# Kernel tuning notes

Hardware: AMD Instinct MI355X
Metric: run time of the kernel (lower is better)

## Reference

```python
import jax, jax.numpy as jnp
import numpy as np
import math

N_HEAD = 16
HEAD_DIM = 64
N_EMBD = 1024
EPS_RMS = 1e-5
U_L2_EPS = 1e-6

def _get_alibi_slopes(n_heads):
    def pow2(n):
        start = 2 ** (-2 ** (-(math.log2(n) - 3)))
        return [start * start ** i for i in range(n)]
    if math.log2(n_heads).is_integer():
        return pow2(n_heads)
    c = 2 ** math.floor(math.log2(n_heads))
    s = pow2(c)
    extra = _get_alibi_slopes(2 * c)
    return s + extra[0::2][: n_heads - c]

def setup_inputs() -> dict:
    key = jax.random.key(0)
    ks = jax.random.split(key, 9)
    B, T = 2, 2048
    H, D, C = N_HEAD, HEAD_DIM, N_EMBD
    x = jax.random.normal(ks[0], (B, T, C), dtype=jnp.float32)
    # Linear weights stored as [in, out] so y = x @ W
    sc = 1.0 / math.sqrt(C)
    Wq = jax.random.normal(ks[1], (C, H * D), dtype=jnp.float32) * sc
    Wk = jax.random.normal(ks[2], (C, H * D), dtype=jnp.float32) * sc
    Wv = jax.random.normal(ks[3], (C, H * D), dtype=jnp.float32) * sc
    Wproj = jax.random.normal(ks[4], (H * D, C), dtype=jnp.float32) * (0.5 / math.sqrt(C) / math.sqrt(12))
    q_rms_w = jnp.ones((D,), dtype=jnp.float32)
    k_rms_w = jnp.ones((D,), dtype=jnp.float32)
    # keygated bias params: omega init = softplus_inverse(1.0), u ~ N(0, 1/sqrt(D))
    omega = jnp.full((H,), math.log(math.expm1(1.0)), dtype=jnp.float32)
    u = jax.random.normal(ks[5], (H, D), dtype=jnp.float32) * (1.0 / math.sqrt(D))
    return {"x": x, "Wq": Wq, "Wk": Wk, "Wv": Wv, "Wproj": Wproj,
            "q_rms_w": q_rms_w, "k_rms_w": k_rms_w, "omega": omega, "u": u}

def _rmsnorm(x, w):
    var = jnp.mean(jnp.square(x), axis=-1, keepdims=True)
    return x * jax.lax.rsqrt(var + EPS_RMS) * w

def reference(x, Wq, Wk, Wv, Wproj, q_rms_w, k_rms_w, omega, u):
    B, T, C = x.shape
    H, D = N_HEAD, HEAD_DIM
    q = (x @ Wq).reshape(B, T, H, D)
    k = (x @ Wk).reshape(B, T, H, D)
    v = (x @ Wv).reshape(B, T, H, D)
    q = _rmsnorm(q, q_rms_w)
    k = _rmsnorm(k, k_rms_w)
    # key-gated additive bias
    slopes = jnp.asarray(_get_alibi_slopes(H), dtype=jnp.float32)  # [H]
    omega_eff = jax.nn.softplus(omega) * slopes                    # [H]
    u_n = u / jnp.maximum(jnp.linalg.norm(u, axis=-1, keepdims=True), U_L2_EPS)
    gate_logits = jnp.einsum('bthd,hd->bht', k, u_n) / math.sqrt(D)  # fp32
    gate = jax.nn.softplus(gate_logits)                            # [B,H,T]
    idx = jnp.arange(T)
    dist = jnp.maximum(idx[:, None] - idx[None, :], 0).astype(jnp.float32)  # [T,T]
    bias = -dist[None, None] * omega_eff[None, :, None, None] * gate[:, :, None, :]  # [B,H,T,T]
    causal = idx[:, None] >= idx[None, :]
    bias = jnp.where(causal[None, None], bias, -jnp.inf)
    # attention
    scale = 1.0 / math.sqrt(D)
    scores = jnp.einsum('bihd,bjhd->bhij', q, k) * scale + bias
    attn = jax.nn.softmax(scores, axis=-1)
    y = jnp.einsum('bhij,bjhd->bihd', attn, v).reshape(B, T, H * D)
    return y @ Wproj
```

## Files before the change

kernel.cpp:

```cpp
#include <hip/hip_runtime.h>
#include <hip/hip_bf16.h>

#define NH 16
#define HD 64
#define CE 1024
#define TT 2048
#define BB 2
#define MR (BB*TT)
#define SWZ(r) ((((r) & 7)) ^ (((r) >> 3) & 3))
#define LOG2E 1.44269504f

typedef __attribute__((ext_vector_type(4))) float f32x4;
typedef __attribute__((ext_vector_type(16))) float f32x16;
typedef __attribute__((ext_vector_type(8))) short s16x8;
typedef unsigned int u32;
typedef unsigned short u16;

__device__ __forceinline__ void gld16(const void* g, void* l) {
  __builtin_amdgcn_global_load_lds((const __attribute__((address_space(1))) unsigned int*)g,
                                   (__attribute__((address_space(3))) unsigned int*)l, 16, 0, 0);
}
__device__ __forceinline__ u16 f2b(float f) {
  union { __hip_bfloat16 b; u16 u; } t;
  t.b = __float2bfloat16(f);
  return t.u;
}
__device__ __forceinline__ u32 pk2(float a, float b) {
  return (u32)f2b(a) | ((u32)f2b(b) << 16);
}
__device__ __forceinline__ float red64_sum(float v) {
#pragma unroll
  for (int m = 1; m < 64; m <<= 1) v += __shfl_xor(v, m, 64);
  return v;
}
__device__ __forceinline__ float softplusf(float x) {
  return x > 20.0f ? x : log1pf(expf(x));
}

__global__ __launch_bounds__(256) void cvt_x(const float* __restrict__ x,
                                             u16* __restrict__ xb, int n4) {
  int stride = gridDim.x * blockDim.x;
  for (int i = blockIdx.x * blockDim.x + threadIdx.x; i < n4; i += stride) {
    float4 v = ((const float4*)x)[i];
    union { u16 u[4]; uint2 p; } o;
    o.u[0] = f2b(v.x); o.u[1] = f2b(v.y); o.u[2] = f2b(v.z); o.u[3] = f2b(v.w);
    ((uint2*)xb)[i] = o.p;
  }
}

__global__ __launch_bounds__(256) void cvt_wt(const float* __restrict__ W0, const float* __restrict__ W1,
                                              const float* __restrict__ W2, const float* __restrict__ W3,
                                              u16* __restrict__ T0, u16* __restrict__ T1,
                                              u16* __restrict__ T2, u16* __restrict__ T3) {
  const float* W = blockIdx.z == 0 ? W0 : blockIdx.z == 1 ? W1 : blockIdx.z == 2 ? W2 : W3;
  u16* T = blockIdx.z == 0 ? T0 : blockIdx.z == 1 ? T1 : blockIdx.z == 2 ? T2 : T3;
  __shared__ float t[64][65];
  int k0 = blockIdx.x * 64, n0 = blockIdx.y * 64;
  int row = threadIdx.x >> 2, seg = threadIdx.x & 3;
#pragma unroll
  for (int i = 0; i < 4; ++i) {
    float4 v = *(const float4*)(W + (size_t)(k0 + row) * CE + n0 + seg * 16 + i * 4);
    int c = seg * 16 + i * 4;
    t[row][c + 0] = v.x; t[row][c + 1] = v.y; t[row][c + 2] = v.z; t[row][c + 3] = v.w;
  }
  __syncthreads();
#pragma unroll
  for (int it = 0; it < 2; ++it) {
    int c = threadIdx.x + it * 256;
    int n = c >> 3, ks = (c & 7) * 8;
    union { u16 u[8]; uint4 p; } o;
#pragma unroll
    for (int e = 0; e < 8; ++e) o.u[e] = f2b(t[ks + e][n]);
    *(uint4*)(T + (size_t)(n0 + n) * CE + k0 + ks) = o.p;
  }
}

#define BM 128
#define BN 128
#define BK 64
__global__ __launch_bounds__(256) void gemm3(const u16* __restrict__ A,
    const u16* __restrict__ B0, const u16* __restrict__ B1,
    const u16* __restrict__ B2,
    float* __restrict__ C0, float* __restrict__ C1, float* __restrict__ C2,
    int M, int N, int K) {
  const u16* Bt = blockIdx.z == 0 ? B0 : blockIdx.z == 1 ? B1 : B2;
  float* C = blockIdx.z == 0 ? C0 : blockIdx.z == 1 ? C1 : C2;
  __shared__ __align__(16) u16 aT[BM * BK];
  __shared__ __align__(16) u16 bT[BN * BK];
  int tid = threadIdx.x;
  int w = tid >> 6, lane = tid & 63, q4 = lane >> 4, r16 = lane & 15;
  int m0 = blockIdx.y * BM, n0 = blockIdx.x * BN;
  int wm = (w >> 1) * 64, wn = (w & 1) * 64;
  f32x4 acc[4][4] = {};
  for (int k0 = 0; k0 < K; k0 += BK) {
#pragma unroll
    for (int it = 0; it < 4; ++it) {
      int c = tid + it * 256;
      int row = c >> 3, sl = c & 7;
      gld16(A + (size_t)(m0 + row) * K + k0 + ((sl ^ SWZ(row)) << 3), &aT[c * 8]);
      gld16(Bt + (size_t)(n0 + row) * K + k0 + ((sl ^ SWZ(row)) << 3), &bT[c * 8]);
    }
    __syncthreads();
#pragma unroll
    for (int kk = 0; kk < 2; ++kk) {
      s16x8 af[4], bfr[4];
#pragma unroll
      for (int i = 0; i < 4; ++i) {
        int ra = wm + i * 16 + r16;
        af[i] = *(const s16x8*)((char*)aT + ra * 128 + ((((kk << 2) | q4) ^ SWZ(ra)) << 4));
        int rb = wn + i * 16 + r16;
        bfr[i] = *(const s16x8*)((char*)bT + rb * 128 + ((((kk << 2) | q4) ^ SWZ(rb)) << 4));
      }
#pragma unroll
      for (int i = 0; i < 4; ++i)
#pragma unroll
        for (int j = 0; j < 4; ++j)
          acc[i][j] = __builtin_amdgcn_mfma_f32_16x16x32_bf16(af[i], bfr[j], acc[i][j], 0, 0, 0);
    }
    __syncthreads();
  }
#pragma unroll
  for (int i = 0; i < 4; ++i)
#pragma unroll
    for (int j = 0; j < 4; ++j)
#pragma unroll
      for (int r = 0; r < 4; ++r) {
        int gm = m0 + wm + i * 16 + (q4 << 2) + r;
        int gn = n0 + wn + j * 16 + r16;
        C[(size_t)gm * N + gn] = acc[i][j][r];
      }
}

__global__ __launch_bounds__(256) void rmsgate(const float* __restrict__ q, const float* __restrict__ k,
    const float* __restrict__ v, const float* __restrict__ qw, const float* __restrict__ kw,
    const float* __restrict__ omega, const float* __restrict__ u,
    u16* __restrict__ qb, u16* __restrict__ kb,
    u16* __restrict__ vtb, float* __restrict__ cg) {
  int b = blockIdx.z, h = blockIdx.y, t0 = blockIdx.x * 64;
  int tid = threadIdx.x, w = tid >> 6, lane = tid & 63;
  float uv = u[h * HD + lane];
  float us = red64_sum(uv * uv);
  float un = uv / fmaxf(sqrtf(us), 1e-6f);
  float qwl = qw[lane], kwl = kw[lane];
  float weff = softplusf(omega[h]) * exp2f(-0.5f * (float)(h + 1)) * LOG2E;
  size_t hb = ((size_t)(b * NH + h)) * TT;
#pragma unroll 4
  for (int it = 0; it < 16; ++it) {
    int t = t0 + w * 16 + it;
    size_t roff = ((size_t)(b * TT + t)) * CE + h * HD + lane;
    float qv = q[roff];
    float rq = rsqrtf(red64_sum(qv * qv) * (1.0f / 64.0f) + 1e-5f);
    qb[(hb + t) * HD + lane] = f2b(qv * rq * qwl * (0.125f * LOG2E));
    float kv = k[roff];
    float rk = rsqrtf(red64_sum(kv * kv) * (1.0f / 64.0f) + 1e-5f);
    float kn = kv * rk * kwl;
    kb[(hb + t) * HD + lane] = f2b(kn);
    float gl = red64_sum(kn * un) * 0.125f;
    if (lane == 0) cg[hb + t] = weff * softplusf(gl);
  }
  __shared__ u16 vt[64 * 65];
  int row = tid >> 2, seg = tid & 3;
#pragma unroll
  for (int i = 0; i < 4; ++i) {
    float4 vv = *(const float4*)(v + ((size_t)(b * TT + t0 + row)) * CE + h * HD + seg * 16 + i * 4);
    int d = seg * 16 + i * 4;
    vt[(d + 0) * 65 + row] = f2b(vv.x);
    vt[(d + 1) * 65 + row] = f2b(vv.y);
    vt[(d + 2) * 65 + row] = f2b(vv.z);
    vt[(d + 3) * 65 + row] = f2b(vv.w);
  }
  __syncthreads();
#pragma unroll
  for (int it = 0; it < 2; ++it) {
    int c = tid + it * 256;
    int d = c >> 3, js = (c & 7) * 8;
    union { u16 u[8]; uint4 p; } o;
#pragma unroll
    for (int e = 0; e < 8; ++e) o.u[e] = vt[d * 65 + js + e];
    *(uint4*)(vtb + (((size_t)(b * NH + h)) * HD + d) * TT + t0 + js) = o.p;
  }
}

#define KVB 64
__global__ __launch_bounds__(64) void attn(const u16* __restrict__ qb,
    const u16* __restrict__ kb, const u16* __restrict__ vtb,
    const float* __restrict__ cg, u16* __restrict__ y) {
  int b = blockIdx.z, h = blockIdx.y;
  int qt = gridDim.x - 1 - blockIdx.x;
  int lane = threadIdx.x & 63;
  int hi = lane >> 5, q5 = lane & 31;
  __shared__ __align__(16) u16 ol[32 * 64];
  size_t hb = ((size_t)(b * NH + h)) * TT;
  size_t vbase = ((size_t)(b * NH + h)) * HD;
  int qrow = qt * 32 + q5;
  const u16* qptr = qb + (hb + qrow) * HD;
  s16x8 qf[4];
#pragma unroll
  for (int kc = 0; kc < 4; ++kc)
    qf[kc] = *(const s16x8*)(qptr + kc * 16 + hi * 8);
  f32x16 accO[2] = {};
  float m = -1e30f, l = 0.f;
  int nt = qt / 2 + 1;
  for (int jt = 0; jt < nt; ++jt) {
    int j0 = jt * KVB;
    const u16* kp0 = kb + (hb + j0 + q5) * HD + hi * 8;
    const u16* kp1 = kb + (hb + j0 + 32 + q5) * HD + hi * 8;
    s16x8 kf0[4], kf1[4];
#pragma unroll
    for (int kc = 0; kc < 4; ++kc) {
      kf0[kc] = *(const s16x8*)(kp0 + kc * 16);
      kf1[kc] = *(const s16x8*)(kp1 + kc * 16);
    }
    const u16* vp0 = vtb + (vbase + q5) * TT + j0 + hi * 8;
    const u16* vp1 = vtb + (vbase + 32 + q5) * TT + j0 + hi * 8;
    s16x8 vfr0[4], vfr1[4];
#pragma unroll
    for (int c = 0; c < 4; ++c) {
      vfr0[c] = *(const s16x8*)(vp0 + c * 16);
      vfr1[c] = *(const s16x8*)(vp1 + c * 16);
    }
    const float* cgp = cg + hb + j0 + 4 * hi;
    f32x4 cgA[4], cgB[4];
#pragma unroll
    for (int g = 0; g < 4; ++g) {
      cgA[g] = *(const f32x4*)(cgp + 8 * g);
      cgB[g] = *(const f32x4*)(cgp + 32 + 8 * g);
    }
    f32x16 s0 = {}, s1 = {};
#pragma unroll
    for (int kc = 0; kc < 4; ++kc) {
      s0 = __builtin_amdgcn_mfma_f32_32x32x16_bf16(kf0[kc], qf[kc], s0, 0, 0, 0);
      s1 = __builtin_amdgcn_mfma_f32_32x32x16_bf16(kf1[kc], qf[kc], s1, 0, 0, 0);
    }
    float dif0 = (float)(qrow - j0);
#pragma unroll
    for (int r = 0; r < 16; ++r) {
      float kvlf = (float)((r & 3) + 8 * (r >> 2) + 4 * hi);
      float d0 = dif0 - kvlf;
      float d1 = d0 - 32.f;
      float cg0 = cgA[r >> 2][r & 3], cg1 = cgB[r >> 2][r & 3];
      s0[r] = (d0 >= 0.f) ? s0[r] - d0 * cg0 : -1e30f;
      s1[r] = (d1 >= 0.f) ? s1[r] - d1 * cg1 : -1e30f;
    }
    float t8[8];
#pragma unroll
    for (int i = 0; i < 8; ++i)
      t8[i] = fmaxf(fmaxf(s0[i], s0[i + 8]), fmaxf(s1[i], s1[i + 8]));
    float t4a = fmaxf(t8[0], t8[4]), t4b = fmaxf(t8[1], t8[5]);
    float t4c = fmaxf(t8[2], t8[6]), t4d = fmaxf(t8[3], t8[7]);
    float pmax = fmaxf(fmaxf(t4a, t4b), fmaxf(t4c, t4d));
    pmax = fmaxf(pmax, __shfl_xor(pmax, 32, 64));
    float mn = fmaxf(m, pmax);
    float al = exp2f(m - mn);
    m = mn;
#pragma unroll
    for (int r = 0; r < 16; ++r) {
      s0[r] = exp2f(s0[r] - m);
      s1[r] = exp2f(s1[r] - m);
    }
    float e8[8];
#pragma unroll
    for (int i = 0; i < 8; ++i)
      e8[i] = (s0[i] + s0[i + 8]) + (s1[i] + s1[i + 8]);
    float e4a = e8[0] + e8[4], e4b = e8[1] + e8[5];
    float e4c = e8[2] + e8[6], e4d = e8[3] + e8[7];
    float ps = (e4a + e4b) + (e4c + e4d);
    ps += __shfl_xor(ps, 32, 64);
    l = l * al + ps;
#pragma unroll
    for (int r = 0; r < 16; ++r) { accO[0][r] *= al; accO[1][r] *= al; }
    auto pvchunk = [&](const f32x16& sc, const s16x8& v00, const s16x8& v01,
                       const s16x8& v10, const s16x8& v11) {
      u32 c01 = pk2(sc[0], sc[1]),  c23 = pk2(sc[2], sc[3]);
      u32 c45 = pk2(sc[4], sc[5]),  c67 = pk2(sc[6], sc[7]);
      u32 c89 = pk2(sc[8], sc[9]),  cAB = pk2(sc[10], sc[11]);
      u32 cCD = pk2(sc[12], sc[13]), cEF = pk2(sc[14], sc[15]);
      u32 x01 = (u32)__shfl_xor((int)c01, 32, 64), x23 = (u32)__shfl_xor((int)c23, 32, 64);
      u32 x45 = (u32)__shfl_xor((int)c45, 32, 64), x67 = (u32)__shfl_xor((int)c67, 32, 64);
      u32 x89 = (u32)__shfl_xor((int)c89, 32, 64), xAB = (u32)__shfl_xor((int)cAB, 32, 64);
      u32 xCD = (u32)__shfl_xor((int)cCD, 32, 64), xEF = (u32)__shfl_xor((int)cEF, 32, 64);
      union { u32 wd[4]; s16x8 v; } Bf0, Bf1;
      Bf0.wd[0] = hi ? x45 : c01; Bf0.wd[1] = hi ? x67 : c23;
      Bf0.wd[2] = hi ? c45 : x01; Bf0.wd[3] = hi ? c67 : x23;
      Bf1.wd[0] = hi ? xCD : c89; Bf1.wd[1] = hi ? xEF : cAB;
      Bf1.wd[2] = hi ? cCD : x89; Bf1.wd[3] = hi ? cEF : xAB;
      accO[0] = __builtin_amdgcn_mfma_f32_32x32x16_bf16(v00, Bf0.v, accO[0], 0, 0, 0);
      accO[0] = __builtin_amdgcn_mfma_f32_32x32x16_bf16(v01, Bf1.v, accO[0], 0, 0, 0);
      accO[1] = __builtin_amdgcn_mfma_f32_32x32x16_bf16(v10, Bf0.v, accO[1], 0, 0, 0);
      accO[1] = __builtin_amdgcn_mfma_f32_32x32x16_bf16(v11, Bf1.v, accO[1], 0, 0, 0);
    };
    pvchunk(s0, vfr0[0], vfr0[1], vfr1[0], vfr1[1]);
    pvchunk(s1, vfr0[2], vfr0[3], vfr1[2], vfr1[3]);
  }
  float inv = 1.f / l;
#pragma unroll
  for (int dt = 0; dt < 2; ++dt)
#pragma unroll
    for (int r = 0; r < 16; ++r) {
      int d = 32 * dt + (r & 3) + 8 * (r >> 2) + 4 * hi;
      *(u16*)((char*)ol + q5 * 128 + (((d >> 3) ^ SWZ(q5)) << 4) + ((d & 7) << 1)) = f2b(accO[dt][r] * inv);
    }
  __syncthreads();
  int row = lane >> 1, half = lane & 1;
#pragma unroll
  for (int s4 = 0; s4 < 4; ++s4) {
    int slot = half * 4 + s4;
    s16x8 vv = *(const s16x8*)((char*)ol + row * 128 + ((slot ^ SWZ(row)) << 4));
    *(s16x8*)(y + ((size_t)(b * TT) + qt * 32 + row) * CE + h * HD + half * 32 + s4 * 8) = vv;
  }
}

extern "C" void kernel_launch(void* const* d_in, const int* in_sizes, int n_in,
                              void* d_out, int out_size, void* d_ws, size_t ws_size,
                              hipStream_t stream) {
  const float* x  = (const float*)d_in[0];
  const float* Wq = (const float*)d_in[1];
  const float* Wk = (const float*)d_in[2];
  const float* Wv = (const float*)d_in[3];
  const float* Wp = (const float*)d_in[4];
  const float* qw = (const float*)d_in[5];
  const float* kw = (const float*)d_in[6];
  const float* om = (const float*)d_in[7];
  const float* u  = (const float*)d_in[8];
  float* out = (float*)d_out;
  char* ws = (char*)d_ws;
  const size_t MB = 1024 * 1024;
  u16* xb  = (u16*)(ws + 0);
  u16* wqt = (u16*)(ws + 8 * MB);
  u16* wkt = (u16*)(ws + 10 * MB);
  u16* wvt = (u16*)(ws + 12 * MB);
  u16* wpt = (u16*)(ws + 14 * MB);
  float* qf = (float*)(ws + 16 * MB);
  float* kf = (float*)(ws + 32 * MB);
  float* vf = (float*)(ws + 48 * MB);
  u16* qbb = (u16*)(ws + 64 * MB);
  u16* kbb = (u16*)(ws + 72 * MB);
  u16* vtb = (u16*)(ws + 80 * MB);
  float* cg = (float*)(ws + 88 * MB);
  u16* yb = (u16*)(ws + 16 * MB);

  cvt_x<<<dim3(2048), dim3(256), 0, stream>>>(x, xb, MR * CE / 4);
  cvt_wt<<<dim3(16, 16, 4), dim3(256), 0, stream>>>(Wq, Wk, Wv, Wp, wqt, wkt, wvt, wpt);
  gemm3<<<dim3(8, 32, 3), dim3(256), 0, stream>>>(xb, wqt, wkt, wvt, qf, kf, vf, MR, CE, CE);
  rmsgate<<<dim3(32, 16, 2), dim3(256), 0, stream>>>(qf, kf, vf, qw, kw, om, u, qbb, kbb, vtb, cg);
  attn<<<dim3(64, 16, 2), dim3(64), 0, stream>>>(qbb, kbb, vtb, cg, yb);
  gemm3<<<dim3(8, 32, 1), dim3(256), 0, stream>>>(yb, wpt, wpt, wpt, out, out, out, MR, CE, CE);
}
```

Measured before the change: 325.7 us.

## Split attention KV loop across two waves with LDS merge, lazy rescale

The attention block now runs two wavefronts, each handling alternating KV tiles of the same 32-row query tile. Their partial softmax states (m, l, O) are merged through shared memory at the end. Other changes: the causal mask runs only on the last tile, the running-max rescale is skipped when the new max stays within a threshold, and the ds shuffles are replaced with permlane32_swap when that builtin exists. The goal is more parallelism and less per-tile ALU work, at the cost of extra LDS use, a block barrier, and possibly lower occupancy.

New measurement: 509.9 us. 1.57x slower.

```diff
diff --git a/kernel.cpp b/kernel.cpp
--- a/kernel.cpp
+++ b/kernel.cpp
@@ -13,6 +13,7 @@
 typedef __attribute__((ext_vector_type(4))) float f32x4;
 typedef __attribute__((ext_vector_type(16))) float f32x16;
 typedef __attribute__((ext_vector_type(8))) short s16x8;
+typedef __attribute__((ext_vector_type(2))) unsigned int u32x2;
 typedef unsigned int u32;
 typedef unsigned short u16;
 
@@ -182,14 +183,18 @@
 }
 
 #define KVB 64
-__global__ __launch_bounds__(64) void attn(const u16* __restrict__ qb,
+__global__ __launch_bounds__(128, 4) void attn(const u16* __restrict__ qb,
     const u16* __restrict__ kb, const u16* __restrict__ vtb,
     const float* __restrict__ cg, u16* __restrict__ y) {
   int b = blockIdx.z, h = blockIdx.y;
   int qt = gridDim.x - 1 - blockIdx.x;
-  int lane = threadIdx.x & 63;
+  int tid = threadIdx.x;
+  int w = tid >> 6;
+  int lane = tid & 63;
   int hi = lane >> 5, q5 = lane & 31;
   __shared__ __align__(16) u16 ol[32 * 64];
+  __shared__ float mO[32][64];
+  __shared__ float mML[2][64];
   size_t hb = ((size_t)(b * NH + h)) * TT;
   size_t vbase = ((size_t)(b * NH + h)) * HD;
   int qrow = qt * 32 + q5;
@@ -201,7 +206,7 @@
   f32x16 accO[2] = {};
   float m = -1e30f, l = 0.f;
   int nt = qt / 2 + 1;
-  for (int jt = 0; jt < nt; ++jt) {
+  for (int jt = w; jt < nt; jt += 2) {
     int j0 = jt * KVB;
     const u16* kp0 = kb + (hb + j0 + q5) * HD + hi * 8;
     const u16* kp1 = kb + (hb + j0 + 32 + q5) * HD + hi * 8;
@@ -232,27 +237,41 @@
       s0 = __builtin_amdgcn_mfma_f32_32x32x16_bf16(kf0[kc], qf[kc], s0, 0, 0, 0);
       s1 = __builtin_amdgcn_mfma_f32_32x32x16_bf16(kf1[kc], qf[kc], s1, 0, 0, 0);
     }
-    float dif0 = (float)(qrow - j0);
-#pragma unroll
-    for (int r = 0; r < 16; ++r) {
-      float kvlf = (float)((r & 3) + 8 * (r >> 2) + 4 * hi);
-      float d0 = dif0 - kvlf;
-      float d1 = d0 - 32.f;
-      float cg0 = cgA[r >> 2][r & 3], cg1 = cgB[r >> 2][r & 3];
-      s0[r] = (d0 >= 0.f) ? s0[r] - d0 * cg0 : -1e30f;
-      s1[r] = (d1 >= 0.f) ? s1[r] - d1 * cg1 : -1e30f;
+    float dif0h = (float)(qrow - j0) - 4.0f * (float)hi;
+    if (jt == nt - 1) {
+#pragma unroll
+      for (int r = 0; r < 16; ++r) {
+        float cr = (float)((r & 3) + 8 * (r >> 2));
+        float d0 = dif0h - cr, d1 = d0 - 32.f;
+        float sv0 = s0[r] - d0 * cgA[r >> 2][r & 3];
+        float sv1 = s1[r] - d1 * cgB[r >> 2][r & 3];
+        s0[r] = (d0 >= 0.f) ? sv0 : -1e30f;
+        s1[r] = (d1 >= 0.f) ? sv1 : -1e30f;
+      }
+    } else {
+#pragma unroll
+      for (int r = 0; r < 16; ++r) {
+        float cr = (float)((r & 3) + 8 * (r >> 2));
+        float d0 = dif0h - cr;
+        s0[r] = s0[r] - d0 * cgA[r >> 2][r & 3];
+        s1[r] = s1[r] - (d0 - 32.f) * cgB[r >> 2][r & 3];
+      }
     }
     float t8[8];
 #pragma unroll
     for (int i = 0; i < 8; ++i)
       t8[i] = fmaxf(fmaxf(s0[i], s0[i + 8]), fmaxf(s1[i], s1[i + 8]));
-    float t4a = fmaxf(t8[0], t8[4]), t4b = fmaxf(t8[1], t8[5]);
-    float t4c = fmaxf(t8[2], t8[6]), t4d = fmaxf(t8[3], t8[7]);
-    float pmax = fmaxf(fmaxf(t4a, t4b), fmaxf(t4c, t4d));
+    float pmax = fmaxf(fmaxf(fmaxf(t8[0], t8[4]), fmaxf(t8[1], t8[5])),
+                       fmaxf(fmaxf(t8[2], t8[6]), fmaxf(t8[3], t8[7])));
     pmax = fmaxf(pmax, __shfl_xor(pmax, 32, 64));
-    float mn = fmaxf(m, pmax);
-    float al = exp2f(m - mn);
-    m = mn;
+    if (!__all(pmax - m <= 11.54f)) {
+      float mn = fmaxf(m, pmax);
+      float al = exp2f(m - mn);
+      m = mn;
+      l *= al;
+#pragma unroll
+      for (int r = 0; r < 16; ++r) { accO[0][r] *= al; accO[1][r] *= al; }
+    }
 #pragma unroll
     for (int r = 0; r < 16; ++r) {
       s0[r] = exp2f(s0[r] - m);
@@ -262,28 +281,33 @@
 #pragma unroll
     for (int i = 0; i < 8; ++i)
       e8[i] = (s0[i] + s0[i + 8]) + (s1[i] + s1[i + 8]);
-    float e4a = e8[0] + e8[4], e4b = e8[1] + e8[5];
-    float e4c = e8[2] + e8[6], e4d = e8[3] + e8[7];
-    float ps = (e4a + e4b) + (e4c + e4d);
+    float ps = ((e8[0] + e8[4]) + (e8[1] + e8[5])) + ((e8[2] + e8[6]) + (e8[3] + e8[7]));
     ps += __shfl_xor(ps, 32, 64);
-    l = l * al + ps;
-#pragma unroll
-    for (int r = 0; r < 16; ++r) { accO[0][r] *= al; accO[1][r] *= al; }
+    l += ps;
     auto pvchunk = [&](const f32x16& sc, const s16x8& v00, const s16x8& v01,
                        const s16x8& v10, const s16x8& v11) {
       u32 c01 = pk2(sc[0], sc[1]),  c23 = pk2(sc[2], sc[3]);
       u32 c45 = pk2(sc[4], sc[5]),  c67 = pk2(sc[6], sc[7]);
       u32 c89 = pk2(sc[8], sc[9]),  cAB = pk2(sc[10], sc[11]);
       u32 cCD = pk2(sc[12], sc[13]), cEF = pk2(sc[14], sc[15]);
+      union { u32 wd[4]; s16x8 v; } Bf0, Bf1;
+#if __has_builtin(__builtin_amdgcn_permlane32_swap)
+      u32x2 sA = __builtin_amdgcn_permlane32_swap(c01, c45, false, false);
+      u32x2 sB = __builtin_amdgcn_permlane32_swap(c23, c67, false, false);
+      u32x2 sC = __builtin_amdgcn_permlane32_swap(c89, cCD, false, false);
+      u32x2 sD = __builtin_amdgcn_permlane32_swap(cAB, cEF, false, false);
+      Bf0.wd[0] = sA.x; Bf0.wd[1] = sB.x; Bf0.wd[2] = sA.y; Bf0.wd[3] = sB.y;
+      Bf1.wd[0] = sC.x; Bf1.wd[1] = sD.x; Bf1.wd[2] = sC.y; Bf1.wd[3] = sD.y;
+#else
       u32 x01 = (u32)__shfl_xor((int)c01, 32, 64), x23 = (u32)__shfl_xor((int)c23, 32, 64);
       u32 x45 = (u32)__shfl_xor((int)c45, 32, 64), x67 = (u32)__shfl_xor((int)c67, 32, 64);
       u32 x89 = (u32)__shfl_xor((int)c89, 32, 64), xAB = (u32)__shfl_xor((int)cAB, 32, 64);
       u32 xCD = (u32)__shfl_xor((int)cCD, 32, 64), xEF = (u32)__shfl_xor((int)cEF, 32, 64);
-      union { u32 wd[4]; s16x8 v; } Bf0, Bf1;
       Bf0.wd[0] = hi ? x45 : c01; Bf0.wd[1] = hi ? x67 : c23;
       Bf0.wd[2] = hi ? c45 : x01; Bf0.wd[3] = hi ? c67 : x23;
       Bf1.wd[0] = hi ? xCD : c89; Bf1.wd[1] = hi ? xEF : cAB;
       Bf1.wd[2] = hi ? cCD : x89; Bf1.wd[3] = hi ? cEF : xAB;
+#endif
       accO[0] = __builtin_amdgcn_mfma_f32_32x32x16_bf16(v00, Bf0.v, accO[0], 0, 0, 0);
       accO[0] = __builtin_amdgcn_mfma_f32_32x32x16_bf16(v01, Bf1.v, accO[0], 0, 0, 0);
       accO[1] = __builtin_amdgcn_mfma_f32_32x32x16_bf16(v10, Bf0.v, accO[1], 0, 0, 0);
@@ -292,15 +316,30 @@
     pvchunk(s0, vfr0[0], vfr0[1], vfr1[0], vfr1[1]);
     pvchunk(s1, vfr0[2], vfr0[3], vfr1[2], vfr1[3]);
   }
-  float inv = 1.f / l;
+  if (w == 1) {
+#pragma unroll
+    for (int r = 0; r < 16; ++r) {
+      mO[r][lane] = accO[0][r];
+      mO[16 + r][lane] = accO[1][r];
+    }
+    mML[0][lane] = m;
+    mML[1][lane] = l;
+  }
+  __syncthreads();
+  if (w == 1) return;
+  float m1 = mML[0][lane], l1 = mML[1][lane];
+  float ms = fmaxf(m, m1);
+  float a0 = exp2f(m - ms), a1 = exp2f(m1 - ms);
+  float lt = l * a0 + l1 * a1;
+  float inv0 = a0 / lt, inv1 = a1 / lt;
 #pragma unroll
   for (int dt = 0; dt < 2; ++dt)
 #pragma unroll
     for (int r = 0; r < 16; ++r) {
+      float val = accO[dt][r] * inv0 + mO[dt * 16 + r][lane] * inv1;
       int d = 32 * dt + (r & 3) + 8 * (r >> 2) + 4 * hi;
-      *(u16*)((char*)ol + q5 * 128 + (((d >> 3) ^ SWZ(q5)) << 4) + ((d & 7) << 1)) = f2b(accO[dt][r] * inv);
-    }
-  __syncthreads();
+      *(u16*)((char*)ol + q5 * 128 + (((d >> 3) ^ SWZ(q5)) << 4) + ((d & 7) << 1)) = f2b(val);
+    }
   int row = lane >> 1, half = lane & 1;
 #pragma unroll
   for (int s4 = 0; s4 < 4; ++s4) {
@@ -343,6 +382,6 @@
   cvt_wt<<<dim3(16, 16, 4), dim3(256), 0, stream>>>(Wq, Wk, Wv, Wp, wqt, wkt, wvt, wpt);
   gemm3<<<dim3(8, 32, 3), dim3(256), 0, stream>>>(xb, wqt, wkt, wvt, qf, kf, vf, MR, CE, CE);
   rmsgate<<<dim3(32, 16, 2), dim3(256), 0, stream>>>(qf, kf, vf, qw, kw, om, u, qbb, kbb, vtb, cg);
-  attn<<<dim3(64, 16, 2), dim3(64), 0, stream>>>(qbb, kbb, vtb, cg, yb);
+  attn<<<dim3(64, 16, 2), dim3(128), 0, stream>>>(qbb, kbb, vtb, cg, yb);
   gemm3<<<dim3(8, 32, 1), dim3(256), 0, stream>>>(yb, wpt, wpt, wpt, out, out, out, MR, CE, CE);
 }
```
